# Kernel tuning notes

Measured on AMD Instinct MI355X. Metric: run time of the kernel, lower is better.

Reference implementation:

```python
import jax, jax.numpy as jnp
import numpy as np

LN_EPS = 1e-5

def _mlp3(x, w1, b1, w2, b2, g, bt, w3, b3):
    # Linear -> ReLU -> Linear -> LayerNorm -> ReLU -> Linear
    h = jax.nn.relu(x @ w1 + b1)
    h = h @ w2 + b2
    mu = jnp.mean(h, axis=-1, keepdims=True)
    var = jnp.mean(jnp.square(h - mu), axis=-1, keepdims=True)
    h = g * (h - mu) * jax.lax.rsqrt(var + LN_EPS) + bt
    h = jax.nn.relu(h)
    return h @ w3 + b3

def _edge_index(B, n):
    # fully connected incl. self-loops, row-major (i, j) per graph, batch-offset
    ij = jnp.arange(n * n)
    i = ij // n
    j = ij % n
    off = (jnp.arange(B) * n)[:, None]
    row = (off + i[None, :]).reshape(-1)  # [B*n*n]
    col = (off + j[None, :]).reshape(-1)
    return row, col

def setup_inputs() -> dict:
    key = jax.random.key(0)
    ks = jax.random.split(key, 16)
    D, H = 512, 512
    B, n = 4096, 7
    s = 0.02
    inp = {
        'states': jax.random.normal(ks[0], (B, n, D), jnp.float32),
        'ew1': jax.random.normal(ks[1], (2 * D, H)) * s, 'eb1': jnp.zeros((H,)),
        'ew2': jax.random.normal(ks[2], (H, H)) * s, 'eb2': jnp.zeros((H,)),
        'eg': jnp.ones((H,)), 'ebt': jnp.zeros((H,)),
        'ew3': jax.random.normal(ks[3], (H, H)) * s, 'eb3': jnp.zeros((H,)),
        'nw1': jax.random.normal(ks[4], (D + H, H)) * s, 'nb1': jnp.zeros((H,)),
        'nw2': jax.random.normal(ks[5], (H, H)) * s, 'nb2': jnp.zeros((H,)),
        'ng': jnp.ones((H,)), 'nbt': jnp.zeros((H,)),
        'nw3': jax.random.normal(ks[6], (H, H)) * s, 'nb3': jnp.zeros((H,)),
        'fnw': jax.random.normal(ks[7], (H, 1)) * s, 'fnb': jnp.zeros((1,)),
        'few': jax.random.normal(ks[8], (H, 1)) * s, 'feb': jnp.zeros((1,)),
    }
    return inp

def reference(states, ew1, eb1, ew2, eb2, eg, ebt, ew3, eb3,
              nw1, nb1, nw2, nb2, ng, nbt, nw3, nb3, fnw, fnb, few, feb):
    B, n, D = states.shape
    node = states.reshape(-1, D)                       # [B*n, D]
    row, col = _edge_index(B, n)                       # [B*n*n]

    def edge_mlp(src, tgt):
        return _mlp3(jnp.concatenate([src, tgt], axis=1),
                     ew1, eb1, ew2, eb2, eg, ebt, ew3, eb3)

    edge_attr = edge_mlp(node[row], node[col])         # [B*n*n, H]
    agg = jax.ops.segment_sum(edge_attr, row, num_segments=B * n)
    node2 = _mlp3(jnp.concatenate([node, agg], axis=1),
                  nw1, nb1, nw2, nb2, ng, nbt, nw3, nb3)
    edge_attr2 = edge_mlp(node2[row], node2[col])

    node_out = (node2 @ fnw + fnb).reshape(B, n)       # unary_preds=1
    edge_out = (edge_attr2 @ few + feb).reshape(B, n * n)
    return jnp.concatenate([node_out, edge_out], axis=1)  # [B, n + n*n]
```

## Files before the change

### kernel.cpp

```cpp
#include <hip/hip_runtime.h>

#define LN_EPS 1e-5f

typedef unsigned short u16;
typedef u16 u16x8 __attribute__((ext_vector_type(8)));
typedef __bf16 bf16x8 __attribute__((ext_vector_type(8)));
typedef float f32x4 __attribute__((ext_vector_type(4)));
typedef float f32x2 __attribute__((ext_vector_type(2)));

__device__ __forceinline__ u16 f2bf(float f){
  return __builtin_bit_cast(u16, (__bf16)f);
}
__device__ __forceinline__ float bf2f(u16 b){
  return (float)__builtin_bit_cast(__bf16, b);
}
__device__ __forceinline__ f32x4 mfma16(u16x8 a, u16x8 b, f32x4 c){
  return __builtin_amdgcn_mfma_f32_16x16x32_bf16(
      __builtin_bit_cast(bf16x8, a), __builtin_bit_cast(bf16x8, b), c, 0, 0, 0);
}
__device__ __forceinline__ int uidx(int row, int k){
  return row * 512 + (k ^ ((row & 7) << 3));
}

__device__ __forceinline__ void zero_acc(f32x4 (&acc)[4][4]){
  #pragma unroll
  for (int mt = 0; mt < 4; ++mt)
    #pragma unroll
    for (int ct = 0; ct < 4; ++ct){
      f32x4 z = {0.f, 0.f, 0.f, 0.f};
      acc[mt][ct] = z;
    }
}

__device__ __forceinline__ void preload_b4(const u16* __restrict__ Bp, int wave, int lane,
                                           u16x8 (&b)[4]){
  const u16* bb = Bp + ((size_t)(wave * 4) * 64 + lane) * 8;
  #pragma unroll
  for (int ct = 0; ct < 4; ++ct) b[ct] = *(const u16x8*)&bb[ct * 512];
}

__device__ __forceinline__ void gemm_pipe(const u16* hA, const u16* __restrict__ Bp,
                                          f32x4 (&acc)[4][4], int wave, int lane,
                                          u16x8 (&b_cur)[4]){
  int lrow = lane & 15, lhi = lane >> 4;
  const u16* bb = Bp + ((size_t)(wave * 4) * 64 + lane) * 8;
  u16x8 b_nxt[4], a[4];
  #pragma unroll
  for (int kt = 0; kt < 16; ++kt){
    #pragma unroll
    for (int mt = 0; mt < 4; ++mt)
      a[mt] = *(const u16x8*)&hA[uidx(mt * 16 + lrow, kt * 32 + lhi * 8)];
    if (kt < 15){
      #pragma unroll
      for (int ct = 0; ct < 4; ++ct)
        b_nxt[ct] = *(const u16x8*)&bb[(size_t)(kt + 1) * 16384 + ct * 512];
    }
    __builtin_amdgcn_s_setprio(1);
    #pragma unroll
    for (int ct = 0; ct < 4; ++ct)
      #pragma unroll
      for (int mt = 0; mt < 4; ++mt)
        acc[mt][ct] = mfma16(a[mt], b_cur[ct], acc[mt][ct]);
    __builtin_amdgcn_s_setprio(0);
    #pragma unroll
    for (int ct = 0; ct < 4; ++ct) b_cur[ct] = b_nxt[ct];
  }
}

__device__ __forceinline__ void gemm_k1024_gA(const u16* __restrict__ A0,
                                              const u16* __restrict__ A1, size_t row0,
                                              const u16* __restrict__ Bp,
                                              f32x4 (&acc)[4][4], int wave, int lane){
  int lrow = lane & 15, lhi = lane >> 4;
  const u16* bb = Bp + ((size_t)(wave * 4) * 64 + lane) * 8;
  const u16* a0 = A0 + (row0 + lrow) * 512 + lhi * 8;
  const u16* a1 = A1 + (row0 + lrow) * 512 + lhi * 8;
  u16x8 b_cur[4], b_nxt[4], a[4];
  #pragma unroll
  for (int ct = 0; ct < 4; ++ct) b_cur[ct] = *(const u16x8*)&bb[ct * 512];
  #pragma unroll
  for (int kt = 0; kt < 32; ++kt){
    const u16* ab = (kt < 16) ? a0 : a1;
    int kk = (kt & 15) * 32;
    #pragma unroll
    for (int mt = 0; mt < 4; ++mt)
      a[mt] = *(const u16x8*)&ab[mt * 8192 + kk];
    if (kt < 31){
      #pragma unroll
      for (int ct = 0; ct < 4; ++ct)
        b_nxt[ct] = *(const u16x8*)&bb[(size_t)(kt + 1) * 16384 + ct * 512];
    }
    __builtin_amdgcn_s_setprio(1);
    #pragma unroll
    for (int ct = 0; ct < 4; ++ct)
      #pragma unroll
      for (int mt = 0; mt < 4; ++mt)
        acc[mt][ct] = mfma16(a[mt], b_cur[ct], acc[mt][ct]);
    __builtin_amdgcn_s_setprio(0);
    #pragma unroll
    for (int ct = 0; ct < 4; ++ct) b_cur[ct] = b_nxt[ct];
  }
}

__device__ __forceinline__ void gemm_pipe_s(const u16* hA, const u16* __restrict__ bbBase,
                                            int ktStride, f32x4 (&acc)[4][4],
                                            int lane){
  int lrow = lane & 15, lhi = lane >> 4;
  u16x8 b_cur[4], b_nxt[4], a[4];
  #pragma unroll
  for (int ct = 0; ct < 4; ++ct) b_cur[ct] = *(const u16x8*)&bbBase[ct * 512];
  #pragma unroll
  for (int kt = 0; kt < 16; ++kt){
    #pragma unroll
    for (int mt = 0; mt < 4; ++mt)
      a[mt] = *(const u16x8*)&hA[uidx(mt * 16 + lrow, kt * 32 + lhi * 8)];
    if (kt < 15){
      #pragma unroll
      for (int ct = 0; ct < 4; ++ct)
        b_nxt[ct] = *(const u16x8*)&bbBase[(size_t)(kt + 1) * ktStride + ct * 512];
    }
    __builtin_amdgcn_s_setprio(1);
    #pragma unroll
    for (int ct = 0; ct < 4; ++ct)
      #pragma unroll
      for (int mt = 0; mt < 4; ++mt)
        acc[mt][ct] = mfma16(a[mt], b_cur[ct], acc[mt][ct]);
    __builtin_amdgcn_s_setprio(0);
    #pragma unroll
    for (int ct = 0; ct < 4; ++ct) b_cur[ct] = b_nxt[ct];
  }
}

__device__ __forceinline__ void add_bias8(f32x4 (&acc)[4][4], const float* __restrict__ b,
                                          int wave, int lane){
  int lrow = lane & 15;
  #pragma unroll
  for (int ct = 0; ct < 4; ++ct){
    float bb = b[wave * 64 + ct * 16 + lrow];
    #pragma unroll
    for (int mt = 0; mt < 4; ++mt)
      #pragma unroll
      for (int r = 0; r < 4; ++r) acc[mt][ct][r] += bb;
  }
}

__device__ __forceinline__ void relu_to_lds(f32x4 (&acc)[4][4], u16* hA,
                                            const float* __restrict__ b,
                                            int wave, int lane){
  int lrow = lane & 15, lhi = lane >> 4;
  #pragma unroll
  for (int ct = 0; ct < 4; ++ct){
    int c = wave * 64 + ct * 16 + lrow;
    float bb = b[c];
    #pragma unroll
    for (int mt = 0; mt < 4; ++mt)
      #pragma unroll
      for (int r = 0; r < 4; ++r){
        int row = mt * 16 + lhi * 4 + r;
        hA[uidx(row, c)] = f2bf(fmaxf(acc[mt][ct][r] + bb, 0.f));
      }
  }
}

template<int TO_ACC>
__device__ __forceinline__ void ln_relu8_t(f32x4 (&acc)[4][4], u16* hA,
    f32x2 (*stats)[8], f32x2* mufb,
    const float* __restrict__ b2, const float* __restrict__ g, const float* __restrict__ bt,
    int wave, int lane, int tid)
{
  int lrow = lane & 15, lhi = lane >> 4;
  float s1[4][4], s2[4][4];
  #pragma unroll
  for (int mt = 0; mt < 4; ++mt)
    #pragma unroll
    for (int r = 0; r < 4; ++r){ s1[mt][r] = 0.f; s2[mt][r] = 0.f; }
  #pragma unroll
  for (int ct = 0; ct < 4; ++ct){
    int c = wave * 64 + ct * 16 + lrow;
    float bb = b2[c];
    #pragma unroll
    for (int mt = 0; mt < 4; ++mt)
      #pragma unroll
      for (int r = 0; r < 4; ++r){
        float x = acc[mt][ct][r] + bb;
        acc[mt][ct][r] = x;
        s1[mt][r] += x; s2[mt][r] += x * x;
      }
  }
  #pragma unroll
  for (int off = 1; off < 16; off <<= 1){
    #pragma unroll
    for (int mt = 0; mt < 4; ++mt)
      #pragma unroll
      for (int r = 0; r < 4; ++r){
        s1[mt][r] += __shfl_xor(s1[mt][r], off);
        s2[mt][r] += __shfl_xor(s2[mt][r], off);
      }
  }
  float sa1 = 0.f, sa2 = 0.f;
  #pragma unroll
  for (int mt = 0; mt < 4; ++mt)
    #pragma unroll
    for (int r = 0; r < 4; ++r)
      if (lrow == mt * 4 + r){ sa1 = s1[mt][r]; sa2 = s2[mt][r]; }
  int rowa = (lrow >> 2) * 16 + lhi * 4 + (lrow & 3);
  f32x2 pa = {sa1, sa2};
  stats[rowa][wave] = pa;
  __syncthreads();
  if (tid < 64){
    float a = 0.f, b = 0.f;
    #pragma unroll
    for (int w = 0; w < 8; ++w){ a += stats[tid][w][0]; b += stats[tid][w][1]; }
    float mu  = a * (1.f / 512.f);
    float var = b * (1.f / 512.f) - mu * mu;
    f32x2 mr = {mu, rsqrtf(fmaxf(var, 0.f) + LN_EPS)};
    mufb[tid] = mr;
  }
  __syncthreads();
  float gv[4], btv[4];
  #pragma unroll
  for (int ct = 0; ct < 4; ++ct){
    int c = wave * 64 + ct * 16 + lrow;
    gv[ct] = g[c]; btv[ct] = bt[c];
  }
  #pragma unroll
  for (int mt = 0; mt < 4; ++mt)
    #pragma unroll
    for (int r = 0; r < 4; ++r){
      int row = mt * 16 + lhi * 4 + r;
      f32x2 mr = mufb[row];
      #pragma unroll
      for (int ct = 0; ct < 4; ++ct){
        int c = wave * 64 + ct * 16 + lrow;
        float x = (acc[mt][ct][r] - mr[0]) * mr[1] * gv[ct] + btv[ct];
        if (TO_ACC) acc[mt][ct][r] = fmaxf(x, 0.f);
        else        hA[uidx(row, c)] = f2bf(fmaxf(x, 0.f));
      }
    }
}

__device__ __forceinline__ void head_partial8(f32x4 (&acc)[4][4], const float* __restrict__ w,
                                              f32x2 (*stats)[8], int wave, int lane)
{
  int lrow = lane & 15, lhi = lane >> 4;
  float hs[4][4];
  #pragma unroll
  for (int mt = 0; mt < 4; ++mt)
    #pragma unroll
    for (int r = 0; r < 4; ++r) hs[mt][r] = 0.f;
  #pragma unroll
  for (int ct = 0; ct < 4; ++ct){
    int c = wave * 64 + ct * 16 + lrow;
    float f = w[c];
    #pragma unroll
    for (int mt = 0; mt < 4; ++mt)
      #pragma unroll
      for (int r = 0; r < 4; ++r) hs[mt][r] += acc[mt][ct][r] * f;
  }
  #pragma unroll
  for (int off = 1; off < 16; off <<= 1)
    #pragma unroll
    for (int mt = 0; mt < 4; ++mt)
      #pragma unroll
      for (int r = 0; r < 4; ++r) hs[mt][r] += __shfl_xor(hs[mt][r], off);
  float sa = 0.f;
  #pragma unroll
  for (int mt = 0; mt < 4; ++mt)
    #pragma unroll
    for (int r = 0; r < 4; ++r)
      if (lrow == mt * 4 + r) sa = hs[mt][r];
  int rowa = (lrow >> 2) * 16 + lhi * 4 + (lrow & 3);
  f32x2 pa = {sa, 0.f};
  stats[rowa][wave] = pa;
}

__device__ __forceinline__ void stage_h1(const u16* __restrict__ PQ, int gg, u16* hA,
                                         int wave, int lane){
  const u16* Pg = PQ + (size_t)gg * 7 * 1024;
  u16x8 pA, qA, pB, qB;
  {
    int e = wave;
    int i = e / 7, j = e % 7;
    pA = *(const u16x8*)&Pg[(size_t)i * 1024 + lane * 8];
    qA = *(const u16x8*)&Pg[(size_t)j * 1024 + 512 + lane * 8];
  }
  #pragma unroll
  for (int it = 0; it < 8; ++it){
    int e = it * 8 + wave;
    if (it < 7){
      int e2 = e + 8;
      if (e2 < 49){
        int i = e2 / 7, j = e2 % 7;
        pB = *(const u16x8*)&Pg[(size_t)i * 1024 + lane * 8];
        qB = *(const u16x8*)&Pg[(size_t)j * 1024 + 512 + lane * 8];
      }
    }
    u16x8 o;
    if (e < 49){
      #pragma unroll
      for (int u = 0; u < 8; ++u)
        o[u] = f2bf(fmaxf(bf2f(pA[u]) + bf2f(qA[u]), 0.f));
    } else {
      #pragma unroll
      for (int u = 0; u < 8; ++u) o[u] = 0;
    }
    *(u16x8*)&hA[uidx(e, lane * 8)] = o;
    pA = pB; qA = qB;
  }
}

__global__ __launch_bounds__(512, 2) void edge0_kernel(
    const u16* __restrict__ PQ, const u16* __restrict__ w2p,
    const float* __restrict__ b2,
    const float* __restrict__ g, const float* __restrict__ bt,
    u16* __restrict__ hsum)
{
  __shared__ alignas(16) u16 hA[64 * 512];
  __shared__ f32x2 stats[64][8];
  __shared__ f32x2 mufb[64];
  int gidx = blockIdx.x;
  int tid = threadIdx.x;
  int wave = tid >> 6, lane = tid & 63;

  stage_h1(PQ, gidx, hA, wave, lane);
  u16x8 bpre[4];
  preload_b4(w2p, wave, lane, bpre);
  __syncthreads();

  f32x4 acc[4][4];
  zero_acc(acc);
  gemm_pipe(hA, w2p, acc, wave, lane, bpre);
  ln_relu8_t<0>(acc, hA, stats, mufb, b2, g, bt, wave, lane, tid);
  __syncthreads();
  {
    int c = tid;
    #pragma unroll
    for (int i = 0; i < 7; ++i){
      float s = 0.f;
      #pragma unroll
      for (int j = 0; j < 7; ++j)
        s += bf2f(hA[uidx(7 * i + j, c)]);
      hsum[((size_t)(gidx * 7 + i)) * 512 + c] = f2bf(s);
    }
  }
}

__global__ __launch_bounds__(512, 2) void edge1_kernel(
    const u16* __restrict__ PQ, const u16* __restrict__ w2p,
    const float* __restrict__ b2,
    const float* __restrict__ g, const float* __restrict__ bt,
    const float* __restrict__ w3f, float* __restrict__ out)
{
  __shared__ alignas(16) u16 hA[64 * 512];
  __shared__ f32x2 stats[64][8];
  __shared__ f32x2 mufb[64];
  int gidx = blockIdx.x;
  int tid = threadIdx.x;
  int wave = tid >> 6, lane = tid & 63;

  stage_h1(PQ, gidx, hA, wave, lane);
  u16x8 bpre[4];
  preload_b4(w2p, wave, lane, bpre);
  __syncthreads();

  f32x4 acc[4][4];
  zero_acc(acc);
  gemm_pipe(hA, w2p, acc, wave, lane, bpre);
  ln_relu8_t<1>(acc, hA, stats, mufb, b2, g, bt, wave, lane, tid);
  head_partial8(acc, w3f, stats, wave, lane);
  __syncthreads();
  if (tid < 49){
    float s = w3f[512];
    #pragma unroll
    for (int w = 0; w < 8; ++w) s += stats[tid][w][0];
    out[(size_t)gidx * 56 + 7 + tid] = s;
  }
}

__global__ __launch_bounds__(512, 2) void node_mega(
    const u16* __restrict__ nodeb, const u16* __restrict__ hsumb,
    const u16* __restrict__ nw1cat, const u16* __restrict__ nw2p,
    const u16* __restrict__ nw3p, const u16* __restrict__ w1p,
    const float* __restrict__ bvec, const float* __restrict__ nb2,
    const float* __restrict__ ng, const float* __restrict__ nbt,
    const float* __restrict__ nb3, const float* __restrict__ hw,
    const float* __restrict__ hb, const float* __restrict__ b1,
    u16* __restrict__ PQ, float* __restrict__ out)
{
  __shared__ alignas(16) u16 hA[64 * 512];
  __shared__ f32x2 stats[64][8];
  __shared__ f32x2 mufb[64];
  int tid = threadIdx.x;
  int wave = tid >> 6, lane = tid & 63;
  int lrow = lane & 15, lhi = lane >> 4;
  size_t row0 = (size_t)blockIdx.x * 64;

  f32x4 acc[4][4];
  zero_acc(acc);
  gemm_k1024_gA(nodeb, hsumb, row0, nw1cat, acc, wave, lane);
  relu_to_lds(acc, hA, bvec, wave, lane);
  u16x8 bpre[4];
  preload_b4(nw2p, wave, lane, bpre);
  __syncthreads();
  zero_acc(acc);
  gemm_pipe(hA, nw2p, acc, wave, lane, bpre);
  ln_relu8_t<0>(acc, hA, stats, mufb, nb2, ng, nbt, wave, lane, tid);
  preload_b4(nw3p, wave, lane, bpre);
  __syncthreads();
  zero_acc(acc);
  gemm_pipe(hA, nw3p, acc, wave, lane, bpre);
  add_bias8(acc, nb3, wave, lane);
  __syncthreads();
  #pragma unroll
  for (int ct = 0; ct < 4; ++ct){
    int c = wave * 64 + ct * 16 + lrow;
    #pragma unroll
    for (int mt = 0; mt < 4; ++mt)
      #pragma unroll
      for (int r = 0; r < 4; ++r)
        hA[uidx(mt * 16 + lhi * 4 + r, c)] = f2bf(acc[mt][ct][r]);
  }
  head_partial8(acc, hw, stats, wave, lane);
  __syncthreads();
  if (tid < 64){
    size_t v = row0 + tid;
    float s = hb[0];
    #pragma unroll
    for (int w = 0; w < 8; ++w) s += stats[tid][w][0];
    out[(v / 7) * 56 + (v % 7)] = s;
  }
  #pragma unroll
  for (int pp = 0; pp < 2; ++pp){
    zero_acc(acc);
    const u16* bbBase = w1p + (((size_t)(pp * 32) + wave * 4) * 64 + lane) * 8;
    gemm_pipe_s(hA, bbBase, 32768, acc, lane);
    #pragma unroll
    for (int ct = 0; ct < 4; ++ct){
      int cc = wave * 64 + ct * 16 + lrow;
      int c = pp * 512 + cc;
      float bb = (pp == 0) ? b1[cc] : 0.f;
      #pragma unroll
      for (int mt = 0; mt < 4; ++mt)
        #pragma unroll
        for (int r = 0; r < 4; ++r){
          size_t grow = row0 + mt * 16 + lhi * 4 + r;
          PQ[grow * 1024 + c] = f2bf(acc[mt][ct][r] + bb);
        }
    }
  }
}

__global__ __launch_bounds__(256, 2) void gemm64_0(
    const u16* __restrict__ A0, const u16* __restrict__ Bp,
    const float* __restrict__ b1, u16* __restrict__ Cout)
{
  int tid = threadIdx.x;
  int wave = tid >> 6, lane = tid & 63;
  int lrow = lane & 15, lhi = lane >> 4;
  size_t row0 = (size_t)blockIdx.x * 64;
  int coff = blockIdx.y * 512;
  const u16* bb = Bp + (((size_t)(coff >> 4) + wave * 8) * 64 + lane) * 8;
  f32x4 acc[4][8];
  #pragma unroll
  for (int mt = 0; mt < 4; ++mt)
    #pragma unroll
    for (int ct = 0; ct < 8; ++ct){
      f32x4 z = {0.f, 0.f, 0.f, 0.f};
      acc[mt][ct] = z;
    }
  u16x8 b_cur[8], b_nxt[8];
  #pragma unroll
  for (int ct = 0; ct < 8; ++ct) b_cur[ct] = *(const u16x8*)&bb[ct * 512];
  #pragma unroll
  for (int kt = 0; kt < 16; ++kt){
    u16x8 af[4];
    #pragma unroll
    for (int mt = 0; mt < 4; ++mt)
      af[mt] = *(const u16x8*)&A0[(row0 + mt * 16 + lrow) * 512 + kt * 32 + lhi * 8];
    if (kt < 15){
      #pragma unroll
      for (int ct = 0; ct < 8; ++ct)
        b_nxt[ct] = *(const u16x8*)&bb[((size_t)(kt + 1) * 64 * 64 + ct * 64) * 8];
    }
    __builtin_amdgcn_s_setprio(1);
    #pragma unroll
    for (int ct = 0; ct < 8; ++ct)
      #pragma unroll
      for (int mt = 0; mt < 4; ++mt) acc[mt][ct] = mfma16(af[mt], b_cur[ct], acc[mt][ct]);
    __builtin_amdgcn_s_setprio(0);
    #pragma unroll
    for (int ct = 0; ct < 8; ++ct) b_cur[ct] = b_nxt[ct];
  }
  #pragma unroll
  for (int ct = 0; ct < 8; ++ct){
    int cc = wave * 128 + ct * 16 + lrow;
    int c = coff + cc;
    float bb2 = (coff == 0) ? b1[cc] : 0.f;
    #pragma unroll
    for (int mt = 0; mt < 4; ++mt)
      #pragma unroll
      for (int r = 0; r < 4; ++r){
        size_t grow = row0 + mt * 16 + lhi * 4 + r;
        Cout[grow * 1024 + c] = f2bf(acc[mt][ct][r] + bb2);
      }
  }
}

__global__ __launch_bounds__(256) void gemm_w3n(
    const float* __restrict__ A, const u16* __restrict__ Bp, u16* __restrict__ dst)
{
  int tid = threadIdx.x;
  int wave = tid >> 6, lane = tid & 63;
  int lrow = lane & 15, lhi = lane >> 4;
  size_t row0 = (size_t)blockIdx.x * 64;
  int coff = blockIdx.y * 128;
  const u16* bb = Bp + (((size_t)(coff >> 4) + wave * 2) * 64 + lane) * 8;
  f32x4 acc[4][2];
  #pragma unroll
  for (int mt = 0; mt < 4; ++mt)
    #pragma unroll
    for (int ct = 0; ct < 2; ++ct){
      f32x4 z = {0.f, 0.f, 0.f, 0.f};
      acc[mt][ct] = z;
    }
  for (int kt = 0; kt < 16; ++kt){
    u16x8 af[4], bv[2];
    #pragma unroll
    for (int mt = 0; mt < 4; ++mt){
      const float* ar = A + (row0 + mt * 16 + lrow) * 512 + kt * 32 + lhi * 8;
      float4 v0 = *(const float4*)ar, v1 = *(const float4*)(ar + 4);
      af[mt][0] = f2bf(v0.x); af[mt][1] = f2bf(v0.y);
      af[mt][2] = f2bf(v0.z); af[mt][3] = f2bf(v0.w);
      af[mt][4] = f2bf(v1.x); af[mt][5] = f2bf(v1.y);
      af[mt][6] = f2bf(v1.z); af[mt][7] = f2bf(v1.w);
    }
    #pragma unroll
    for (int ct = 0; ct < 2; ++ct)
      bv[ct] = *(const u16x8*)&bb[(size_t)kt * 16384 + ct * 512];
    #pragma unroll
    for (int ct = 0; ct < 2; ++ct)
      #pragma unroll
      for (int mt = 0; mt < 4; ++mt) acc[mt][ct] = mfma16(af[mt], bv[ct], acc[mt][ct]);
  }
  #pragma unroll
  for (int ct = 0; ct < 2; ++ct){
    int c = coff + wave * 32 + ct * 16 + lrow;
    int ctp = c >> 4, lanelo = c & 15;
    #pragma unroll
    for (int mt = 0; mt < 4; ++mt)
      #pragma unroll
      for (int r = 0; r < 4; ++r){
        int k = (int)row0 + mt * 16 + lhi * 4 + r;
        int kt = k >> 5, lanehi = (k >> 3) & 3, j = k & 7;
        dst[((size_t)(kt * 32 + ctp) * 64 + lanehi * 16 + lanelo) * 8 + j]
            = f2bf(acc[mt][ct][r]);
      }
  }
}

__device__ __forceinline__ void pack_body(const float* __restrict__ W, u16* __restrict__ dst,
                                          int N, int w1mode, int idx){
  int lane = idx & 63;
  int t = idx >> 6;
  int nt = N >> 4;
  int ct = t % nt;
  int kt = t / nt;
  int c  = ct * 16 + (lane & 15);
  int k0 = kt * 32 + (lane >> 4) * 8;
  u16x8 o;
  #pragma unroll
  for (int j = 0; j < 8; ++j){
    int k = k0 + j;
    float v;
    if (w1mode){
      v = (c < 512) ? W[(size_t)k * 512 + c] : W[(size_t)(k + 512) * 512 + (c - 512)];
    } else {
      v = W[(size_t)k * N + c];
    }
    o[j] = f2bf(v);
  }
  *(u16x8*)&dst[(size_t)idx * 8] = o;
}

__global__ __launch_bounds__(256) void prep_all(
    const float* __restrict__ states,
    const float* __restrict__ ew1, const float* __restrict__ nw1,
    const float* __restrict__ ew2, const float* __restrict__ nw2,
    const float* __restrict__ nw3, const float* __restrict__ ew3,
    const float* __restrict__ few, const float* __restrict__ eb3,
    const float* __restrict__ feb, const float* __restrict__ nb1,
    u16* __restrict__ nodeb, u16* __restrict__ w1p, u16* __restrict__ nw1cat,
    u16* __restrict__ nw1bp, u16* __restrict__ w2p, u16* __restrict__ nw2p,
    u16* __restrict__ nw3p, float* __restrict__ w3f, float* __restrict__ bvec)
{
  int blk = blockIdx.x;
  int tid = threadIdx.x;
  if (blk < 256){
    pack_body(ew1, w1p, 1024, 1, blk * 256 + tid);
  } else if (blk < 384){
    pack_body(nw1, nw1cat, 512, 0, (blk - 256) * 256 + tid);
  } else if (blk < 512){
    pack_body(nw1 + 512 * 512, nw1bp, 512, 0, (blk - 384) * 256 + tid);
  } else if (blk < 640){
    pack_body(ew2, w2p, 512, 0, (blk - 512) * 256 + tid);
  } else if (blk < 768){
    pack_body(nw2, nw2p, 512, 0, (blk - 640) * 256 + tid);
  } else if (blk < 896){
    pack_body(nw3, nw3p, 512, 0, (blk - 768) * 256 + tid);
  } else if (blk < 1025){
    int k = (blk - 896) * 4 + (tid >> 6);
    int l = tid & 63;
    if (k <= 512){
      const float* row = (k < 512) ? (ew3 + (size_t)k * 512) : eb3;
      float s = 0.f;
      for (int c = l; c < 512; c += 64) s += row[c] * few[c];
      #pragma unroll
      for (int off = 32; off; off >>= 1) s += __shfl_down(s, off);
      if (l == 0) w3f[k] = (k < 512) ? s : s + feb[0];
    }
  } else if (blk < 1027){
    int c = (blk - 1025) * 256 + tid;
    float s = 0.f;
    for (int m = 0; m < 512; ++m)
      s += eb3[m] * nw1[(size_t)(512 + m) * 512 + c];
    bvec[c] = nb1[c] + 7.f * s;
  } else {
    int idx = (blk - 1027) * 256 + tid;
    const float4* s = (const float4*)states;
    float4 a = s[(size_t)idx * 2], b = s[(size_t)idx * 2 + 1];
    u16x8 o;
    o[0] = f2bf(a.x); o[1] = f2bf(a.y); o[2] = f2bf(a.z); o[3] = f2bf(a.w);
    o[4] = f2bf(b.x); o[5] = f2bf(b.y); o[6] = f2bf(b.z); o[7] = f2bf(b.w);
    *(u16x8*)&nodeb[(size_t)idx * 8] = o;
  }
}

extern "C" void kernel_launch(void* const* d_in, const int* in_sizes, int n_in,
                              void* d_out, int out_size, void* d_ws, size_t ws_size,
                              hipStream_t stream)
{
  (void)in_sizes; (void)n_in; (void)out_size; (void)ws_size;
  const float* states = (const float*)d_in[0];
  const float* ew1 = (const float*)d_in[1];
  const float* eb1 = (const float*)d_in[2];
  const float* ew2 = (const float*)d_in[3];
  const float* eb2 = (const float*)d_in[4];
  const float* eg  = (const float*)d_in[5];
  const float* ebt = (const float*)d_in[6];
  const float* ew3 = (const float*)d_in[7];
  const float* eb3 = (const float*)d_in[8];
  const float* nw1 = (const float*)d_in[9];
  const float* nb1 = (const float*)d_in[10];
  const float* nw2 = (const float*)d_in[11];
  const float* nb2 = (const float*)d_in[12];
  const float* ng  = (const float*)d_in[13];
  const float* nbt = (const float*)d_in[14];
  const float* nw3 = (const float*)d_in[15];
  const float* nb3 = (const float*)d_in[16];
  const float* fnw = (const float*)d_in[17];
  const float* fnb = (const float*)d_in[18];
  const float* few = (const float*)d_in[19];
  const float* feb = (const float*)d_in[20];
  float* out = (float*)d_out;

  char* ws = (char*)d_ws;
  size_t off = 0;
  auto alloc = [&](size_t bytes) -> void* {
    void* p = ws + off;
    off += (bytes + 255) & ~(size_t)255;
    return p;
  };
  const size_t NV = 28672;
  u16* PQ     = (u16*)alloc(NV * 1024 * 2);
  u16* nodeb  = (u16*)alloc(NV * 512 * 2);
  u16* hsumb  = (u16*)alloc(NV * 512 * 2);
  u16* w1p    = (u16*)alloc(512 * 1024 * 2);
  u16* nw1cat = (u16*)alloc(1024 * 512 * 2);
  u16* nw1bp  = (u16*)alloc(512 * 512 * 2);
  u16* w2p    = (u16*)alloc(512 * 512 * 2);
  u16* nw2p   = (u16*)alloc(512 * 512 * 2);
  u16* nw3p   = (u16*)alloc(512 * 512 * 2);
  float* w3f  = (float*)alloc(513 * 4);
  float* bvec = (float*)alloc(512 * 4);

  prep_all<<<1027 + 7168, 256, 0, stream>>>(
      states, ew1, nw1, ew2, nw2, nw3, ew3, few, eb3, feb, nb1,
      nodeb, w1p, nw1cat, nw1bp, w2p, nw2p, nw3p, w3f, bvec);
  gemm_w3n<<<dim3(8, 4), 256, 0, stream>>>(ew3, nw1bp, nw1cat + 512 * 512);

  gemm64_0<<<dim3(448, 2), 256, 0, stream>>>(nodeb, w1p, eb1, PQ);
  edge0_kernel<<<4096, 512, 0, stream>>>(PQ, w2p, eb2, eg, ebt, hsumb);
  node_mega<<<448, 512, 0, stream>>>(nodeb, hsumb, nw1cat, nw2p, nw3p, w1p,
                                     bvec, nb2, ng, nbt, nb3, fnw, fnb, eb1, PQ, out);
  edge1_kernel<<<4096, 512, 0, stream>>>(PQ, w2p, eb2, eg, ebt, w3f, out);
}
```

Measured before the change: 556.4 us.

## Pack nine source nodes per edge block to fill 64-row MFMA tiles

```diff
diff --git a/kernel.cpp b/kernel.cpp
--- a/kernel.cpp
+++ b/kernel.cpp
@@ -1,6 +1,10 @@
 #include <hip/hip_runtime.h>
 
 #define LN_EPS 1e-5f
+#define NSRC 28672
+#define SPB 9
+#define EPB 63
+#define NB_E 3186
 
 typedef unsigned short u16;
 typedef u16 u16x8 __attribute__((ext_vector_type(8)));
@@ -274,29 +278,37 @@
   stats[rowa][wave] = pa;
 }
 
-__device__ __forceinline__ void stage_h1(const u16* __restrict__ PQ, int gg, u16* hA,
+__device__ __forceinline__ void stage_h1(const u16* __restrict__ PQ, int bs, u16* hA,
                                          int wave, int lane){
-  const u16* Pg = PQ + (size_t)gg * 7 * 1024;
   u16x8 pA, qA, pB, qB;
+  bool vA = false, vB;
   {
     int e = wave;
-    int i = e / 7, j = e % 7;
-    pA = *(const u16x8*)&Pg[(size_t)i * 1024 + lane * 8];
-    qA = *(const u16x8*)&Pg[(size_t)j * 1024 + 512 + lane * 8];
+    int sl = e / 7, j = e % 7;
+    int s = bs + sl;
+    vA = (s < NSRC);
+    if (vA){
+      int qn = s - s % 7 + j;
+      pA = *(const u16x8*)&PQ[(size_t)s * 1024 + lane * 8];
+      qA = *(const u16x8*)&PQ[(size_t)qn * 1024 + 512 + lane * 8];
+    }
   }
   #pragma unroll
   for (int it = 0; it < 8; ++it){
     int e = it * 8 + wave;
     if (it < 7){
       int e2 = e + 8;
-      if (e2 < 49){
-        int i = e2 / 7, j = e2 % 7;
-        pB = *(const u16x8*)&Pg[(size_t)i * 1024 + lane * 8];
-        qB = *(const u16x8*)&Pg[(size_t)j * 1024 + 512 + lane * 8];
+      int sl = e2 / 7, j = e2 % 7;
+      int s = bs + sl;
+      vB = (e2 < EPB) && (s < NSRC);
+      if (vB){
+        int qn = s - s % 7 + j;
+        pB = *(const u16x8*)&PQ[(size_t)s * 1024 + lane * 8];
+        qB = *(const u16x8*)&PQ[(size_t)qn * 1024 + 512 + lane * 8];
       }
     }
     u16x8 o;
-    if (e < 49){
+    if (vA){
       #pragma unroll
       for (int u = 0; u < 8; ++u)
         o[u] = f2bf(fmaxf(bf2f(pA[u]) + bf2f(qA[u]), 0.f));
@@ -305,7 +317,7 @@
       for (int u = 0; u < 8; ++u) o[u] = 0;
     }
     *(u16x8*)&hA[uidx(e, lane * 8)] = o;
-    pA = pB; qA = qB;
+    pA = pB; qA = qB; vA = vB;
   }
 }
 
@@ -318,11 +330,11 @@
   __shared__ alignas(16) u16 hA[64 * 512];
   __shared__ f32x2 stats[64][8];
   __shared__ f32x2 mufb[64];
-  int gidx = blockIdx.x;
+  int bs = blockIdx.x * SPB;
   int tid = threadIdx.x;
   int wave = tid >> 6, lane = tid & 63;
 
-  stage_h1(PQ, gidx, hA, wave, lane);
+  stage_h1(PQ, bs, hA, wave, lane);
   u16x8 bpre[4];
   preload_b4(w2p, wave, lane, bpre);
   __syncthreads();
@@ -333,14 +345,24 @@
   ln_relu8_t<0>(acc, hA, stats, mufb, b2, g, bt, wave, lane, tid);
   __syncthreads();
   {
-    int c = tid;
-    #pragma unroll
-    for (int i = 0; i < 7; ++i){
-      float s = 0.f;
-      #pragma unroll
-      for (int j = 0; j < 7; ++j)
-        s += bf2f(hA[uidx(7 * i + j, c)]);
-      hsum[((size_t)(gidx * 7 + i)) * 512 + c] = f2bf(s);
+    int c0 = lane * 8;
+    for (int sl = wave; sl < SPB; sl += 8){
+      int s = bs + sl;
+      if (s < NSRC){
+        float a8[8];
+        #pragma unroll
+        for (int u = 0; u < 8; ++u) a8[u] = 0.f;
+        #pragma unroll
+        for (int j = 0; j < 7; ++j){
+          u16x8 v = *(const u16x8*)&hA[uidx(sl * 7 + j, c0)];
+          #pragma unroll
+          for (int u = 0; u < 8; ++u) a8[u] += bf2f(v[u]);
+        }
+        u16x8 o;
+        #pragma unroll
+        for (int u = 0; u < 8; ++u) o[u] = f2bf(a8[u]);
+        *(u16x8*)&hsum[(size_t)s * 512 + c0] = o;
+      }
     }
   }
 }
@@ -354,11 +376,11 @@
   __shared__ alignas(16) u16 hA[64 * 512];
   __shared__ f32x2 stats[64][8];
   __shared__ f32x2 mufb[64];
-  int gidx = blockIdx.x;
+  int bs = blockIdx.x * SPB;
   int tid = threadIdx.x;
   int wave = tid >> 6, lane = tid & 63;
 
-  stage_h1(PQ, gidx, hA, wave, lane);
+  stage_h1(PQ, bs, hA, wave, lane);
   u16x8 bpre[4];
   preload_b4(w2p, wave, lane, bpre);
   __syncthreads();
@@ -369,11 +391,16 @@
   ln_relu8_t<1>(acc, hA, stats, mufb, b2, g, bt, wave, lane, tid);
   head_partial8(acc, w3f, stats, wave, lane);
   __syncthreads();
-  if (tid < 49){
-    float s = w3f[512];
-    #pragma unroll
-    for (int w = 0; w < 8; ++w) s += stats[tid][w][0];
-    out[(size_t)gidx * 56 + 7 + tid] = s;
+  if (tid < EPB){
+    int sl = tid / 7, j = tid % 7;
+    int s = bs + sl;
+    if (s < NSRC){
+      int gg = s / 7, i = s % 7;
+      float sum = w3f[512];
+      #pragma unroll
+      for (int w = 0; w < 8; ++w) sum += stats[tid][w][0];
+      out[(size_t)gg * 56 + 7 + i * 7 + j] = sum;
+    }
   }
 }
 
@@ -689,8 +716,8 @@
   gemm_w3n<<<dim3(8, 4), 256, 0, stream>>>(ew3, nw1bp, nw1cat + 512 * 512);
 
   gemm64_0<<<dim3(448, 2), 256, 0, stream>>>(nodeb, w1p, eb1, PQ);
-  edge0_kernel<<<4096, 512, 0, stream>>>(PQ, w2p, eb2, eg, ebt, hsumb);
+  edge0_kernel<<<NB_E, 512, 0, stream>>>(PQ, w2p, eb2, eg, ebt, hsumb);
   node_mega<<<448, 512, 0, stream>>>(nodeb, hsumb, nw1cat, nw2p, nw3p, w1p,
                                      bvec, nb2, ng, nbt, nb3, fnw, fnb, eb1, PQ, out);
-  edge1_kernel<<<4096, 512, 0, stream>>>(PQ, w2p, eb2, eg, ebt, w3f, out);
-}
+  edge1_kernel<<<NB_E, 512, 0, stream>>>(PQ, w2p, eb2, eg, ebt, w3f, out);
+}
```

Result: faster. 539.0 us (-3.1%).
